# Kernel optimization log

Hardware: AMD Instinct MI355X
Metric: run time of the kernel (lower is better)

The kernel has to match this reference:

```python
import jax, jax.numpy as jnp
import numpy as np


def setup_inputs() -> dict:
    key = jax.random.key(0)
    kq, kk, kv, kb = jax.random.split(key, 4)
    B, H, S, D = 4, 16, 1024, 64
    return {
        "query": jax.random.normal(kq, (B, H, S, D), dtype=jnp.float32),
        "key": jax.random.normal(kk, (B, H, S, D), dtype=jnp.float32),
        "value": jax.random.normal(kv, (B, H, S, D), dtype=jnp.float32),
        "bias_mask": jax.random.normal(kb, (1, 1, S, S), dtype=jnp.float32),
    }


def reference(query, key, value, bias_mask):
    d_k = query.shape[-1]
    scale = 1.0 / jnp.sqrt(jnp.asarray(d_k, dtype=query.dtype))
    # scores: [B, H, Sq, Sk]
    scores = jnp.einsum("bhqd,bhkd->bhqk", query, key) * scale
    scores = scores + bias_mask
    attn_weights = jax.nn.softmax(scores, axis=-1)
    output = jnp.einsum("bhqk,bhkd->bhqd", attn_weights, value)
    return (output, attn_weights)
```

## Files before the change

kernel.cpp:

```cpp
#include <hip/hip_runtime.h>

constexpr int SEQ = 1024;
constexpr int DH  = 64;
constexpr int QR  = 32;
constexpr int KT  = 128;
constexpr int KS  = 72;
constexpr int VS  = 136;
constexpr int PS  = 136;

typedef __bf16 bf16x8 __attribute__((ext_vector_type(8)));
typedef __bf16 bf16x4 __attribute__((ext_vector_type(4)));
typedef float  f32x4  __attribute__((ext_vector_type(4)));

__global__ __launch_bounds__(256, 3)
void attn_flash_kernel(const float* __restrict__ Q, const float* __restrict__ K,
                       const float* __restrict__ V, const float* __restrict__ bias,
                       float* __restrict__ out, float* __restrict__ attn)
{
    __shared__ __bf16 sQ[QR * KS];
    __shared__ __bf16 sK[KT * KS];
    __shared__ __bf16 sV[DH * VS];
    __shared__ __bf16 sP[QR * PS];
    __shared__ float  sRM[2][QR];
    __shared__ float  sRL[2][QR];

    const int tid  = threadIdx.x;
    const int w    = tid >> 6;
    const int l    = tid & 63;
    const int qt   = w & 1;
    const int ch   = w >> 1;
    const int lm   = l & 15;
    const int lq   = l >> 4;
    const int head = blockIdx.x >> 5;
    const int q0   = (blockIdx.x & 31) * QR;
    const float scale = 0.125f;

    const float* Qh = Q + (size_t)head * SEQ * DH;
    const float* Kh = K + (size_t)head * SEQ * DH;
    const float* Vh = V + (size_t)head * SEQ * DH;
    float* outh  = out  + (size_t)head * SEQ * DH;
    float* attnh = attn + (size_t)head * SEQ * SEQ;

    #pragma unroll
    for (int i = 0; i < 2; ++i) {
        int u = tid + 256 * i;
        int row = u >> 4, dg = u & 15;
        f32x4 v = *(const f32x4*)(Qh + (size_t)(q0 + row) * DH + dg * 4);
        bf16x4 b;
        b[0] = (__bf16)v[0]; b[1] = (__bf16)v[1]; b[2] = (__bf16)v[2]; b[3] = (__bf16)v[3];
        *(bf16x4*)(sQ + row * KS + dg * 4) = b;
    }

    const int rowg = q0 + qt * 16 + lq * 4;

    float m_run[4], l_run[4];
    #pragma unroll
    for (int r = 0; r < 4; ++r) { m_run[r] = -1e30f; l_run[r] = 0.f; }

    for (int kt = 0; kt < SEQ / KT; ++kt) {
        __syncthreads();
        #pragma unroll
        for (int i = 0; i < 8; ++i) {
            int u = tid + 256 * i;
            int row = u >> 4, dg = u & 15;
            f32x4 v = *(const f32x4*)(Kh + (size_t)(kt * KT + row) * DH + dg * 4);
            bf16x4 b;
            b[0] = (__bf16)v[0]; b[1] = (__bf16)v[1]; b[2] = (__bf16)v[2]; b[3] = (__bf16)v[3];
            *(bf16x4*)(sK + row * KS + dg * 4) = b;
        }
        __syncthreads();

        f32x4 acc[4] = {{0,0,0,0},{0,0,0,0},{0,0,0,0},{0,0,0,0}};
        #pragma unroll
        for (int ks = 0; ks < 2; ++ks) {
            bf16x8 afrag = *(const bf16x8*)(sQ + (qt * 16 + lm) * KS + ks * 32 + lq * 8);
            #pragma unroll
            for (int c = 0; c < 4; ++c) {
                bf16x8 bfrag = *(const bf16x8*)(sK + ((ch * 4 + c) * 16 + lm) * KS + ks * 32 + lq * 8);
                acc[c] = __builtin_amdgcn_mfma_f32_16x16x32_bf16(afrag, bfrag, acc[c], 0, 0, 0);
            }
        }
        const int colg = kt * KT + ch * 64 + lm;
        #pragma unroll
        for (int r = 0; r < 4; ++r) {
            const float* brow = bias + (size_t)(rowg + r) * SEQ + colg;
            float x0 = acc[0][r] * scale + brow[0];
            float x1 = acc[1][r] * scale + brow[16];
            float x2 = acc[2][r] * scale + brow[32];
            float x3 = acc[3][r] * scale + brow[48];
            float tm = fmaxf(fmaxf(x0, x1), fmaxf(x2, x3));
            #pragma unroll
            for (int off = 1; off < 16; off <<= 1)
                tm = fmaxf(tm, __shfl_xor(tm, off));
            float mn = fmaxf(m_run[r], tm);
            float corr = __expf(m_run[r] - mn);
            float s = __expf(x0 - mn) + __expf(x1 - mn) + __expf(x2 - mn) + __expf(x3 - mn);
            #pragma unroll
            for (int off = 1; off < 16; off <<= 1)
                s += __shfl_xor(s, off);
            l_run[r] = l_run[r] * corr + s;
            m_run[r] = mn;
        }
    }

    if (lm == 0) {
        #pragma unroll
        for (int r = 0; r < 4; ++r) {
            sRM[ch][qt * 16 + lq * 4 + r] = m_run[r];
            sRL[ch][qt * 16 + lq * 4 + r] = l_run[r];
        }
    }
    __syncthreads();
    float mfin[4], linv[4];
    #pragma unroll
    for (int r = 0; r < 4; ++r) {
        int row = qt * 16 + lq * 4 + r;
        float m0 = sRM[0][row], m1 = sRM[1][row];
        float m  = fmaxf(m0, m1);
        float lsum = sRL[0][row] * __expf(m0 - m) + sRL[1][row] * __expf(m1 - m);
        mfin[r] = m;
        linv[r] = 1.0f / lsum;
    }

    const int dtb = ch * 2;
    f32x4 oacc[2] = {{0,0,0,0},{0,0,0,0}};

    for (int kt = 0; kt < SEQ / KT; ++kt) {
        __syncthreads();
        #pragma unroll
        for (int i = 0; i < 8; ++i) {
            int u = tid + 256 * i;
            int row = u >> 4, dg = u & 15;
            f32x4 v = *(const f32x4*)(Kh + (size_t)(kt * KT + row) * DH + dg * 4);
            bf16x4 b;
            b[0] = (__bf16)v[0]; b[1] = (__bf16)v[1]; b[2] = (__bf16)v[2]; b[3] = (__bf16)v[3];
            *(bf16x4*)(sK + row * KS + dg * 4) = b;
        }
        #pragma unroll
        for (int i = 0; i < 2; ++i) {
            int u = tid + 256 * i;
            int kb = u & 31, db = u >> 5;
            int k0 = kb * 4, d0 = db * 4;
            f32x4 v0 = *(const f32x4*)(Vh + (size_t)(kt * KT + k0 + 0) * DH + d0);
            f32x4 v1 = *(const f32x4*)(Vh + (size_t)(kt * KT + k0 + 1) * DH + d0);
            f32x4 v2 = *(const f32x4*)(Vh + (size_t)(kt * KT + k0 + 2) * DH + d0);
            f32x4 v3 = *(const f32x4*)(Vh + (size_t)(kt * KT + k0 + 3) * DH + d0);
            #pragma unroll
            for (int jj = 0; jj < 4; ++jj) {
                bf16x4 b;
                b[0] = (__bf16)v0[jj]; b[1] = (__bf16)v1[jj];
                b[2] = (__bf16)v2[jj]; b[3] = (__bf16)v3[jj];
                *(bf16x4*)(sV + (d0 + jj) * VS + k0) = b;
            }
        }
        __syncthreads();

        f32x4 acc[4] = {{0,0,0,0},{0,0,0,0},{0,0,0,0},{0,0,0,0}};
        #pragma unroll
        for (int ks = 0; ks < 2; ++ks) {
            bf16x8 afrag = *(const bf16x8*)(sQ + (qt * 16 + lm) * KS + ks * 32 + lq * 8);
            #pragma unroll
            for (int c = 0; c < 4; ++c) {
                bf16x8 bfrag = *(const bf16x8*)(sK + ((ch * 4 + c) * 16 + lm) * KS + ks * 32 + lq * 8);
                acc[c] = __builtin_amdgcn_mfma_f32_16x16x32_bf16(afrag, bfrag, acc[c], 0, 0, 0);
            }
        }
        const int colg = kt * KT + ch * 64 + lm;
        const int colt = ch * 64 + lm;
        #pragma unroll
        for (int r = 0; r < 4; ++r) {
            const float* brow = bias + (size_t)(rowg + r) * SEQ + colg;
            float* arow = attnh + (size_t)(rowg + r) * SEQ + colg;
            float il = linv[r], mf = mfin[r];
            #pragma unroll
            for (int c = 0; c < 4; ++c) {
                float x = acc[c][r] * scale + brow[c * 16];
                float p = __expf(x - mf) * il;
                arow[c * 16] = p;
                sP[(qt * 16 + lq * 4 + r) * PS + colt + c * 16] = (__bf16)p;
            }
        }
        __syncthreads();

        #pragma unroll
        for (int ks = 0; ks < 4; ++ks) {
            bf16x8 afrag = *(const bf16x8*)(sP + (qt * 16 + lm) * PS + ks * 32 + lq * 8);
            #pragma unroll
            for (int c = 0; c < 2; ++c) {
                bf16x8 bfrag = *(const bf16x8*)(sV + ((dtb + c) * 16 + lm) * VS + ks * 32 + lq * 8);
                oacc[c] = __builtin_amdgcn_mfma_f32_16x16x32_bf16(afrag, bfrag, oacc[c], 0, 0, 0);
            }
        }
    }

    #pragma unroll
    for (int c = 0; c < 2; ++c)
        #pragma unroll
        for (int r = 0; r < 4; ++r)
            outh[(size_t)(rowg + r) * DH + (dtb + c) * 16 + lm] = oacc[c][r];
}

extern "C" void kernel_launch(void* const* d_in, const int* in_sizes, int n_in,
                              void* d_out, int out_size, void* d_ws, size_t ws_size,
                              hipStream_t stream) {
    const float* Q    = (const float*)d_in[0];
    const float* K    = (const float*)d_in[1];
    const float* V    = (const float*)d_in[2];
    const float* bias = (const float*)d_in[3];
    float* out  = (float*)d_out;
    float* attn = (float*)d_out + 4 * 16 * 1024 * 64;
    dim3 grid(64 * (SEQ / QR));
    dim3 block(256);
    attn_flash_kernel<<<grid, block, 0, stream>>>(Q, K, V, bias, out, attn);
}
```

Measured before the change: 469.4 us.

## Cache scores in registers, double-buffer K/V with register prefetch

```diff
diff --git a/kernel.cpp b/kernel.cpp
--- a/kernel.cpp
+++ b/kernel.cpp
@@ -4,23 +4,25 @@
 constexpr int DH  = 64;
 constexpr int QR  = 32;
 constexpr int KT  = 128;
+constexpr int NKT = SEQ / KT;
 constexpr int KS  = 72;
 constexpr int VS  = 136;
 constexpr int PS  = 136;
 
+constexpr int BUF = 26112;
+constexpr int SPOFF = 17408;
+
 typedef __bf16 bf16x8 __attribute__((ext_vector_type(8)));
 typedef __bf16 bf16x4 __attribute__((ext_vector_type(4)));
 typedef float  f32x4  __attribute__((ext_vector_type(4)));
 
-__global__ __launch_bounds__(256, 3)
+__global__ __launch_bounds__(256, 2)
 void attn_flash_kernel(const float* __restrict__ Q, const float* __restrict__ K,
                        const float* __restrict__ V, const float* __restrict__ bias,
                        float* __restrict__ out, float* __restrict__ attn)
 {
+    __shared__ __align__(16) char smem[2 * BUF];
     __shared__ __bf16 sQ[QR * KS];
-    __shared__ __bf16 sK[KT * KS];
-    __shared__ __bf16 sV[DH * VS];
-    __shared__ __bf16 sP[QR * PS];
     __shared__ float  sRM[2][QR];
     __shared__ float  sRL[2][QR];
 
@@ -31,8 +33,8 @@
     const int ch   = w >> 1;
     const int lm   = l & 15;
     const int lq   = l >> 4;
-    const int head = blockIdx.x >> 5;
-    const int q0   = (blockIdx.x & 31) * QR;
+    const int head = blockIdx.x & 63;
+    const int q0   = (blockIdx.x >> 6) * QR;
     const float scale = 0.125f;
 
     const float* Qh = Q + (size_t)head * SEQ * DH;
@@ -41,53 +43,84 @@
     float* outh  = out  + (size_t)head * SEQ * DH;
     float* attnh = attn + (size_t)head * SEQ * SEQ;
 
+    const int srow = tid >> 4;
+    const int sdg  = tid & 15;
+
+    f32x4 kv[8];
+    #pragma unroll
+    for (int i = 0; i < 8; ++i)
+        kv[i] = *(const f32x4*)(Kh + (size_t)(srow + 16 * i) * DH + sdg * 4);
+
     #pragma unroll
     for (int i = 0; i < 2; ++i) {
-        int u = tid + 256 * i;
-        int row = u >> 4, dg = u & 15;
-        f32x4 v = *(const f32x4*)(Qh + (size_t)(q0 + row) * DH + dg * 4);
+        int row = srow + 16 * i;
+        f32x4 v = *(const f32x4*)(Qh + (size_t)(q0 + row) * DH + sdg * 4);
         bf16x4 b;
         b[0] = (__bf16)v[0]; b[1] = (__bf16)v[1]; b[2] = (__bf16)v[2]; b[3] = (__bf16)v[3];
-        *(bf16x4*)(sQ + row * KS + dg * 4) = b;
+        *(bf16x4*)(sQ + row * KS + sdg * 4) = b;
     }
 
     const int rowg = q0 + qt * 16 + lq * 4;
 
+    f32x4 xs[NKT][4];
     float m_run[4], l_run[4];
     #pragma unroll
     for (int r = 0; r < 4; ++r) { m_run[r] = -1e30f; l_run[r] = 0.f; }
 
-    for (int kt = 0; kt < SEQ / KT; ++kt) {
+    bf16x8 aQ0, aQ1;
+
+    #pragma unroll
+    for (int kt = 0; kt < NKT; ++kt) {
+        __bf16* sK = (__bf16*)(smem + (kt & 1) * BUF);
+        #pragma unroll
+        for (int i = 0; i < 8; ++i) {
+            bf16x4 b;
+            b[0] = (__bf16)kv[i][0]; b[1] = (__bf16)kv[i][1];
+            b[2] = (__bf16)kv[i][2]; b[3] = (__bf16)kv[i][3];
+            *(bf16x4*)(sK + (srow + 16 * i) * KS + sdg * 4) = b;
+        }
         __syncthreads();
-        #pragma unroll
-        for (int i = 0; i < 8; ++i) {
-            int u = tid + 256 * i;
-            int row = u >> 4, dg = u & 15;
-            f32x4 v = *(const f32x4*)(Kh + (size_t)(kt * KT + row) * DH + dg * 4);
-            bf16x4 b;
-            b[0] = (__bf16)v[0]; b[1] = (__bf16)v[1]; b[2] = (__bf16)v[2]; b[3] = (__bf16)v[3];
-            *(bf16x4*)(sK + row * KS + dg * 4) = b;
-        }
-        __syncthreads();
-
-        f32x4 acc[4] = {{0,0,0,0},{0,0,0,0},{0,0,0,0},{0,0,0,0}};
-        #pragma unroll
-        for (int ks = 0; ks < 2; ++ks) {
-            bf16x8 afrag = *(const bf16x8*)(sQ + (qt * 16 + lm) * KS + ks * 32 + lq * 8);
-            #pragma unroll
-            for (int c = 0; c < 4; ++c) {
-                bf16x8 bfrag = *(const bf16x8*)(sK + ((ch * 4 + c) * 16 + lm) * KS + ks * 32 + lq * 8);
-                acc[c] = __builtin_amdgcn_mfma_f32_16x16x32_bf16(afrag, bfrag, acc[c], 0, 0, 0);
-            }
+
+        if (kt < NKT - 1) {
+            #pragma unroll
+            for (int i = 0; i < 8; ++i)
+                kv[i] = *(const f32x4*)(Kh + (size_t)((kt + 1) * KT + srow + 16 * i) * DH + sdg * 4);
         }
         const int colg = kt * KT + ch * 64 + lm;
+        float bb[4][4];
         #pragma unroll
         for (int r = 0; r < 4; ++r) {
             const float* brow = bias + (size_t)(rowg + r) * SEQ + colg;
-            float x0 = acc[0][r] * scale + brow[0];
-            float x1 = acc[1][r] * scale + brow[16];
-            float x2 = acc[2][r] * scale + brow[32];
-            float x3 = acc[3][r] * scale + brow[48];
+            bb[r][0] = brow[0]; bb[r][1] = brow[16]; bb[r][2] = brow[32]; bb[r][3] = brow[48];
+        }
+
+        if (kt == 0) {
+            aQ0 = *(const bf16x8*)(sQ + (qt * 16 + lm) * KS + 0 * 32 + lq * 8);
+            aQ1 = *(const bf16x8*)(sQ + (qt * 16 + lm) * KS + 1 * 32 + lq * 8);
+        }
+
+        #pragma unroll
+        for (int c = 0; c < 4; ++c) xs[kt][c] = (f32x4){0.f, 0.f, 0.f, 0.f};
+        __builtin_amdgcn_s_setprio(1);
+        #pragma unroll
+        for (int c = 0; c < 4; ++c) {
+            bf16x8 bfrag = *(const bf16x8*)(sK + ((ch * 4 + c) * 16 + lm) * KS + 0 * 32 + lq * 8);
+            xs[kt][c] = __builtin_amdgcn_mfma_f32_16x16x32_bf16(aQ0, bfrag, xs[kt][c], 0, 0, 0);
+        }
+        #pragma unroll
+        for (int c = 0; c < 4; ++c) {
+            bf16x8 bfrag = *(const bf16x8*)(sK + ((ch * 4 + c) * 16 + lm) * KS + 1 * 32 + lq * 8);
+            xs[kt][c] = __builtin_amdgcn_mfma_f32_16x16x32_bf16(aQ1, bfrag, xs[kt][c], 0, 0, 0);
+        }
+        __builtin_amdgcn_s_setprio(0);
+
+        #pragma unroll
+        for (int r = 0; r < 4; ++r) {
+            float x0 = xs[kt][0][r] * scale + bb[r][0];
+            float x1 = xs[kt][1][r] * scale + bb[r][1];
+            float x2 = xs[kt][2][r] * scale + bb[r][2];
+            float x3 = xs[kt][3][r] * scale + bb[r][3];
+            xs[kt][0][r] = x0; xs[kt][1][r] = x1; xs[kt][2][r] = x2; xs[kt][3][r] = x3;
             float tm = fmaxf(fmaxf(x0, x1), fmaxf(x2, x3));
             #pragma unroll
             for (int off = 1; off < 16; off <<= 1)
@@ -110,7 +143,19 @@
             sRL[ch][qt * 16 + lq * 4 + r] = l_run[r];
         }
     }
+
+    const int vkb  = tid & 31;
+    const int vdb0 = tid >> 5;
+    f32x4 vv[2][4];
+    #pragma unroll
+    for (int i = 0; i < 2; ++i) {
+        #pragma unroll
+        for (int j = 0; j < 4; ++j)
+            vv[i][j] = *(const f32x4*)(Vh + (size_t)(vkb * 4 + j) * DH + (vdb0 + 8 * i) * 4);
+    }
+
     __syncthreads();
+
     float mfin[4], linv[4];
     #pragma unroll
     for (int r = 0; r < 4; ++r) {
@@ -125,63 +170,48 @@
     const int dtb = ch * 2;
     f32x4 oacc[2] = {{0,0,0,0},{0,0,0,0}};
 
-    for (int kt = 0; kt < SEQ / KT; ++kt) {
-        __syncthreads();
-        #pragma unroll
-        for (int i = 0; i < 8; ++i) {
-            int u = tid + 256 * i;
-            int row = u >> 4, dg = u & 15;
-            f32x4 v = *(const f32x4*)(Kh + (size_t)(kt * KT + row) * DH + dg * 4);
-            bf16x4 b;
-            b[0] = (__bf16)v[0]; b[1] = (__bf16)v[1]; b[2] = (__bf16)v[2]; b[3] = (__bf16)v[3];
-            *(bf16x4*)(sK + row * KS + dg * 4) = b;
-        }
+    #pragma unroll
+    for (int kt = 0; kt < NKT; ++kt) {
+        __bf16* sV = (__bf16*)(smem + (kt & 1) * BUF);
+        __bf16* sP = (__bf16*)(smem + (kt & 1) * BUF + SPOFF);
+
         #pragma unroll
         for (int i = 0; i < 2; ++i) {
-            int u = tid + 256 * i;
-            int kb = u & 31, db = u >> 5;
-            int k0 = kb * 4, d0 = db * 4;
-            f32x4 v0 = *(const f32x4*)(Vh + (size_t)(kt * KT + k0 + 0) * DH + d0);
-            f32x4 v1 = *(const f32x4*)(Vh + (size_t)(kt * KT + k0 + 1) * DH + d0);
-            f32x4 v2 = *(const f32x4*)(Vh + (size_t)(kt * KT + k0 + 2) * DH + d0);
-            f32x4 v3 = *(const f32x4*)(Vh + (size_t)(kt * KT + k0 + 3) * DH + d0);
+            int k0 = vkb * 4, d0 = (vdb0 + 8 * i) * 4;
             #pragma unroll
             for (int jj = 0; jj < 4; ++jj) {
                 bf16x4 b;
-                b[0] = (__bf16)v0[jj]; b[1] = (__bf16)v1[jj];
-                b[2] = (__bf16)v2[jj]; b[3] = (__bf16)v3[jj];
+                b[0] = (__bf16)vv[i][0][jj]; b[1] = (__bf16)vv[i][1][jj];
+                b[2] = (__bf16)vv[i][2][jj]; b[3] = (__bf16)vv[i][3][jj];
                 *(bf16x4*)(sV + (d0 + jj) * VS + k0) = b;
             }
         }
-        __syncthreads();
-
-        f32x4 acc[4] = {{0,0,0,0},{0,0,0,0},{0,0,0,0},{0,0,0,0}};
-        #pragma unroll
-        for (int ks = 0; ks < 2; ++ks) {
-            bf16x8 afrag = *(const bf16x8*)(sQ + (qt * 16 + lm) * KS + ks * 32 + lq * 8);
-            #pragma unroll
-            for (int c = 0; c < 4; ++c) {
-                bf16x8 bfrag = *(const bf16x8*)(sK + ((ch * 4 + c) * 16 + lm) * KS + ks * 32 + lq * 8);
-                acc[c] = __builtin_amdgcn_mfma_f32_16x16x32_bf16(afrag, bfrag, acc[c], 0, 0, 0);
-            }
-        }
+
         const int colg = kt * KT + ch * 64 + lm;
         const int colt = ch * 64 + lm;
         #pragma unroll
         for (int r = 0; r < 4; ++r) {
-            const float* brow = bias + (size_t)(rowg + r) * SEQ + colg;
             float* arow = attnh + (size_t)(rowg + r) * SEQ + colg;
             float il = linv[r], mf = mfin[r];
             #pragma unroll
             for (int c = 0; c < 4; ++c) {
-                float x = acc[c][r] * scale + brow[c * 16];
-                float p = __expf(x - mf) * il;
-                arow[c * 16] = p;
+                float p = __expf(xs[kt][c][r] - mf) * il;
+                __builtin_nontemporal_store(p, arow + c * 16);
                 sP[(qt * 16 + lq * 4 + r) * PS + colt + c * 16] = (__bf16)p;
             }
         }
         __syncthreads();
 
+        if (kt < NKT - 1) {
+            #pragma unroll
+            for (int i = 0; i < 2; ++i) {
+                #pragma unroll
+                for (int j = 0; j < 4; ++j)
+                    vv[i][j] = *(const f32x4*)(Vh + (size_t)((kt + 1) * KT + vkb * 4 + j) * DH + (vdb0 + 8 * i) * 4);
+            }
+        }
+
+        __builtin_amdgcn_s_setprio(1);
         #pragma unroll
         for (int ks = 0; ks < 4; ++ks) {
             bf16x8 afrag = *(const bf16x8*)(sP + (qt * 16 + lm) * PS + ks * 32 + lq * 8);
@@ -191,13 +221,15 @@
                 oacc[c] = __builtin_amdgcn_mfma_f32_16x16x32_bf16(afrag, bfrag, oacc[c], 0, 0, 0);
             }
         }
+        __builtin_amdgcn_s_setprio(0);
     }
 
     #pragma unroll
     for (int c = 0; c < 2; ++c)
         #pragma unroll
         for (int r = 0; r < 4; ++r)
-            outh[(size_t)(rowg + r) * DH + (dtb + c) * 16 + lm] = oacc[c][r];
+            __builtin_nontemporal_store(oacc[c][r],
+                outh + (size_t)(rowg + r) * DH + (dtb + c) * 16 + lm);
 }
 
 extern "C" void kernel_launch(void* const* d_in, const int* in_sizes, int n_in,
```

Result: faster. 437.1 us (-6.9%).
